# Kernel tuning notes

Hardware: AMD Instinct MI355X
Metric: run time of the kernel (lower is better)

The kernel has to match this reference:

```python
import jax, jax.numpy as jnp
import numpy as np

D = 3  # hardcoded window half-width in the module


def setup_inputs() -> dict:
    key = jax.random.key(0)
    ks = jax.random.split(key, 5)
    B, T, S = 16, 1024, 4096
    q_size, c_size, p_size = 512, 512, 512
    q = jax.random.normal(ks[0], (B, q_size, S), jnp.float32)
    c_t = jax.random.normal(ks[1], (B, T, c_size), jnp.float32)
    # torch nn.Linear weight layouts: (out_features, in_features)
    W_a = jax.random.normal(ks[2], (c_size, q_size), jnp.float32) / np.sqrt(q_size).astype(np.float32)
    W_p = jax.random.normal(ks[3], (p_size, c_size), jnp.float32) / np.sqrt(c_size).astype(np.float32)
    V_p = jax.random.normal(ks[4], (1, p_size), jnp.float32) / np.sqrt(p_size).astype(np.float32)
    return {"q": q, "c_t": c_t, "W_a": W_a, "W_p": W_p, "V_p": V_p}


def reference(q, c_t, W_a, W_p, V_p):
    B, q_size, S = q.shape
    # predictive alignment: p_t = S * sigmoid(V_p tanh(W_p c_t)) -> (B, T, 1)
    p_t = S * jax.nn.sigmoid(jnp.tanh(c_t @ W_p.T) @ V_p.T)
    # pad one NaN column at the front of the sequence, then (B, S+1, q_size)
    q_pad = jnp.pad(q, ((0, 0), (0, 0), (1, 0)), constant_values=jnp.nan).transpose(0, 2, 1)
    # window indices: clamp(long(p_t) + idx + 1, 0, S+1) % (S+1), idx in [-D, D]
    offsets = jnp.arange(-D + 1, D + 2)  # (2D+1,)
    s = jnp.clip(p_t.astype(jnp.int32) + offsets[None, None, :], 0, S + 1) % (S + 1)  # (B,T,2D+1)
    # per-batch gather of the local window: (B, T, 2D+1, q_size)
    qg = q_pad[jnp.arange(B)[:, None, None], s]
    nan_loc = jnp.isnan(qg[..., 0])  # (B, T, 2D+1)
    qg = jnp.where(nan_loc[..., None], 0.0, qg)
    # score: dot(W_a q, c_t) -> (B, T, 2D+1)
    a_t = jnp.einsum('btwq,cq,btc->btw', qg, W_a, c_t)
    a_t = jnp.where(nan_loc, -jnp.inf, a_t)
    attn = jax.nn.softmax(a_t, axis=2)
    # Gaussian decay around predicted position p_t
    gauss = jnp.exp(-2.0 * ((jnp.clip(s.astype(jnp.float32) - 1.0, 0.0, None) - p_t) / D) ** 2)
    W_attn = attn * gauss
    out = jnp.einsum('btw,btwq->btq', W_attn, qg)  # (B, T, q_size)
    return out
```

## Files before the change

### kernel.cpp

```cpp
#include <hip/hip_runtime.h>
#include <hip/hip_bf16.h>

#define BB 16
#define TT 1024
#define SS 4096
#define CS 512
#define QS 512
#define PS 512
#define NROW (BB*TT)

typedef unsigned short ushort_t;
typedef unsigned int u32;
typedef short bf16x8 __attribute__((ext_vector_type(8)));
typedef float f32x4 __attribute__((ext_vector_type(4)));

#define AS1 __attribute__((address_space(1)))
#define AS3 __attribute__((address_space(3)))

__device__ __forceinline__ void gl2l16(const void* g, void* l) {
    __builtin_amdgcn_global_load_lds((const AS1 u32*)g, (AS3 u32*)l, 16, 0, 0);
}

__device__ __forceinline__ ushort_t f2bf(float f) {
    u32 x = __float_as_uint(f);
    return (ushort_t)((x + 0x7fffu + ((x >> 16) & 1u)) >> 16);
}
__device__ __forceinline__ float bf2f(ushort_t b) {
    return __uint_as_float(((u32)b) << 16);
}

__global__ __launch_bounds__(256) void k_conv(const float* __restrict__ c,
                                              const float* __restrict__ Wa,
                                              const float* __restrict__ Wp,
                                              ushort_t* __restrict__ A,
                                              ushort_t* __restrict__ B,
                                              int* __restrict__ cnt,
                                              int* __restrict__ hist,
                                              int* __restrict__ cur) {
    const int blk = blockIdx.x;
    const int t = threadIdx.x;
    if (blk < 8192) {
        const int i = blk * 256 + t;
        const int m = i >> 7;
        const int k = (i & 127) * 4;
        float4 v = *(const float4*)(c + (size_t)m * CS + k);
        ushort4 hi, lo;
        hi.x = f2bf(v.x); lo.x = f2bf(v.x - bf2f(hi.x));
        hi.y = f2bf(v.y); lo.y = f2bf(v.y - bf2f(hi.y));
        hi.z = f2bf(v.z); lo.z = f2bf(v.z - bf2f(hi.z));
        hi.w = f2bf(v.w); lo.w = f2bf(v.w - bf2f(hi.w));
        *(ushort4*)(A + (size_t)m * 1024 + k)       = hi;
        *(ushort4*)(A + (size_t)m * 1024 + 512 + k) = lo;
    } else if (blk < 9216) {
        const int n = blk - 8192;
        if (n == 0 && t < 2) cnt[t] = 0;
        #pragma unroll
        for (int kk = 0; kk < 2; ++kk) {
            const int k = t + 256 * kk;
            float v = (n < 512) ? Wa[(size_t)k * QS + n] : Wp[(size_t)(n - 512) * CS + k];
            ushort_t hi = f2bf(v);
            ushort_t lo = f2bf(v - bf2f(hi));
            B[(size_t)n * 1024 + k]       = hi;
            B[(size_t)n * 1024 + 512 + k] = lo;
        }
    } else {
        const int idx = (blk - 9216) * 256 + t;
        if (idx < 2048) hist[idx] = 0;
        else cur[idx - 2048] = 0;
    }
}

__global__ __launch_bounds__(1024, 4) void k_gemm(const ushort_t* __restrict__ A,
                                                  const ushort_t* __restrict__ B,
                                                  const float* __restrict__ V_p,
                                                  float* __restrict__ u,
                                                  float* __restrict__ zpart) {
    __shared__ ushort_t lds[8][8192];
    const int tid = threadIdx.x;
    const int l = tid & 63;
    const int w = tid >> 6;
    const int wm = w >> 2;
    const int wn = w & 3;
    const int ln = l & 15, lh = l >> 4;

    const int orig = blockIdx.x;
    const int swz = ((orig & 7) << 5) + (orig >> 3);
    const int m0 = (swz >> 2) * 256;
    const int nt = swz & 3;
    const int n0 = nt * 256;

    const int srow = tid >> 2;
    const int scg  = tid & 3;
    const int scol0 = (scg ^ ((srow >> 1) & 3)) * 8;

    const int swzr = (lh ^ ((ln >> 1) & 3)) << 3;
    int aoffL[4], boffL[4];
    #pragma unroll
    for (int mi = 0; mi < 4; ++mi)
        aoffL[mi] = (wm * 64 + mi * 16 + ln) * 32 + swzr;
    #pragma unroll
    for (int ni = 0; ni < 4; ++ni)
        boffL[ni] = (wn * 64 + ni * 16 + ln) * 32 + swzr;

    f32x4 acc[4][4];
    #pragma unroll
    for (int a = 0; a < 4; ++a)
        #pragma unroll
        for (int b2 = 0; b2 < 4; ++b2) acc[a][b2] = (f32x4){0.f, 0.f, 0.f, 0.f};

    auto STAGE = [&](int c) {
        const int tt = c >> 2, rem = c & 3, kh = rem >> 1;
        const int blk = tt >> 3, k0 = (tt & 7) << 6;
        const ushort_t* src;
        if (rem & 1) {
            const int boff = (blk == 1) ? 512 : 0;
            src = B + (size_t)(n0 + srow) * 1024 + boff + k0 + kh * 32 + scol0;
        } else {
            const int aoff = (blk == 2) ? 512 : 0;
            src = A + (size_t)(m0 + srow) * 1024 + aoff + k0 + kh * 32 + scol0;
        }
        gl2l16(src, &lds[c & 7][tid * 8]);
    };

    #pragma unroll
    for (int c = 0; c < 4; ++c) STAGE(c);
    asm volatile("s_waitcnt vmcnt(0)" ::: "memory");
    __builtin_amdgcn_s_barrier();

    #pragma unroll 1
    for (int t = 0; t < 24; ++t) {
        if (t < 23) {
            #pragma unroll
            for (int i = 0; i < 4; ++i) STAGE(4 * t + 4 + i);
        }
        {
            const ushort_t* bA = &lds[(4 * t) & 7][0];
            const ushort_t* bB = &lds[(4 * t + 1) & 7][0];
            bf16x8 af[4], bb[4];
            #pragma unroll
            for (int mi = 0; mi < 4; ++mi)
                af[mi] = *(const bf16x8*)(bA + aoffL[mi]);
            #pragma unroll
            for (int ni = 0; ni < 4; ++ni)
                bb[ni] = *(const bf16x8*)(bB + boffL[ni]);
            __builtin_amdgcn_s_setprio(1);
            #pragma unroll
            for (int mi = 0; mi < 4; ++mi)
                #pragma unroll
                for (int ni = 0; ni < 4; ++ni)
                    acc[mi][ni] = __builtin_amdgcn_mfma_f32_16x16x32_bf16(
                        af[mi], bb[ni], acc[mi][ni], 0, 0, 0);
            __builtin_amdgcn_s_setprio(0);
        }
        {
            const ushort_t* bA = &lds[(4 * t + 2) & 7][0];
            const ushort_t* bB = &lds[(4 * t + 3) & 7][0];
            bf16x8 af[4], bb[4];
            #pragma unroll
            for (int mi = 0; mi < 4; ++mi)
                af[mi] = *(const bf16x8*)(bA + aoffL[mi]);
            #pragma unroll
            for (int ni = 0; ni < 4; ++ni)
                bb[ni] = *(const bf16x8*)(bB + boffL[ni]);
            __builtin_amdgcn_s_setprio(1);
            #pragma unroll
            for (int mi = 0; mi < 4; ++mi)
                #pragma unroll
                for (int ni = 0; ni < 4; ++ni)
                    acc[mi][ni] = __builtin_amdgcn_mfma_f32_16x16x32_bf16(
                        af[mi], bb[ni], acc[mi][ni], 0, 0, 0);
            __builtin_amdgcn_s_setprio(0);
        }
        asm volatile("s_waitcnt vmcnt(0)" ::: "memory");
        __builtin_amdgcn_s_barrier();
    }

    if (nt < 2) {
        #pragma unroll
        for (int mi = 0; mi < 4; ++mi) {
            #pragma unroll
            for (int r = 0; r < 4; ++r) {
                const int m = m0 + wm * 64 + mi * 16 + lh * 4 + r;
                float* up = u + (size_t)m * QS + nt * 256 + wn * 64 + ln;
                #pragma unroll
                for (int ni = 0; ni < 4; ++ni) up[ni * 16] = acc[mi][ni][r];
            }
        }
    } else {
        float vp[4];
        #pragma unroll
        for (int ni = 0; ni < 4; ++ni)
            vp[ni] = V_p[(nt - 2) * 256 + wn * 64 + ni * 16 + ln];
        #pragma unroll
        for (int mi = 0; mi < 4; ++mi) {
            #pragma unroll
            for (int r = 0; r < 4; ++r) {
                float sv = 0.f;
                #pragma unroll
                for (int ni = 0; ni < 4; ++ni) sv += tanhf(acc[mi][ni][r]) * vp[ni];
                sv += __shfl_xor(sv, 1, 64);
                sv += __shfl_xor(sv, 2, 64);
                sv += __shfl_xor(sv, 4, 64);
                sv += __shfl_xor(sv, 8, 64);
                if (ln == 0)
                    zpart[(size_t)(m0 + wm * 64 + mi * 16 + lh * 4 + r) * 8 +
                          (nt - 2) * 4 + wn] = sv;
            }
        }
    }
}

__global__ __launch_bounds__(256) void k_z(const float* __restrict__ zpart,
                                           float* __restrict__ pt, int* __restrict__ tr,
                                           int* __restrict__ list1, int* __restrict__ cnt1) {
    const int row = blockIdx.x * 256 + threadIdx.x;
    const float4 a = *(const float4*)(zpart + (size_t)row * 8);
    const float4 b = *(const float4*)(zpart + (size_t)row * 8 + 4);
    float z = ((a.x + a.y) + (a.z + a.w)) + ((b.x + b.y) + (b.z + b.w));
    float ptv = 4096.f / (1.f + expf(-z));
    float fr = ptv - floorf(ptv);
    pt[row] = ptv;
    tr[row] = (int)ptv;
    if (fr < 0.06f || fr > 0.94f) {
        int i = atomicAdd(cnt1, 1);
        list1[i] = row;
    }
}

__global__ __launch_bounds__(256) void k_rep1(
    const float* __restrict__ c_t, const float* __restrict__ W_p,
    const float* __restrict__ V_p, float* __restrict__ pt, int* __restrict__ tr,
    const int* __restrict__ list1, const int* __restrict__ cnt1,
    int* __restrict__ list2, int* __restrict__ cnt2)
{
    const int tid = threadIdx.x;
    const int lane = tid & 63;
    const int wid = tid >> 6;
    const int n1 = cnt1[0];
    __shared__ float cl[8][132 * 4];
    __shared__ double zl[4][8];
    __shared__ int rows_s[8];

    for (int g0 = blockIdx.x * 8; g0 < n1; g0 += gridDim.x * 8) {
        const int nr = min(8, n1 - g0);
        __syncthreads();
        if (tid < nr) rows_s[tid] = list1[g0 + tid];
        __syncthreads();
        for (int idx = tid; idx < nr * 128; idx += 256) {
            int r = idx >> 7, k = (idx & 127) * 4;
            *(float4*)&cl[r][k] = *(const float4*)(c_t + (size_t)rows_s[r] * CS + k);
        }
        __syncthreads();

        const float* wp0 = W_p + (size_t)tid * CS;
        const float* wp1 = W_p + (size_t)(tid + 256) * CS;
        f32x4 acc[2][8];
        #pragma unroll
        for (int p = 0; p < 2; ++p)
            #pragma unroll
            for (int r = 0; r < 8; ++r) acc[p][r] = (f32x4){0.f, 0.f, 0.f, 0.f};

        for (int k = 0; k < CS; k += 16) {
            f32x4 w0[4], w1[4];
            #pragma unroll
            for (int j = 0; j < 4; ++j) {
                w0[j] = *(const f32x4*)(wp0 + k + 4 * j);
                w1[j] = *(const f32x4*)(wp1 + k + 4 * j);
            }
            #pragma unroll
            for (int j = 0; j < 4; ++j) {
                #pragma unroll
                for (int r = 0; r < 8; ++r) {
                    f32x4 c4 = *(const f32x4*)&cl[r][k + 4 * j];
                    acc[0][r] += c4 * w0[j];
                    acc[1][r] += c4 * w1[j];
                }
            }
        }

        const float vp0 = V_p[tid];
        const float vp1 = V_p[tid + 256];
        double zp[8];
        #pragma unroll
        for (int r = 0; r < 8; ++r) {
            float X0 = (acc[0][r][0] + acc[0][r][1]) + (acc[0][r][2] + acc[0][r][3]);
            float X1 = (acc[1][r][0] + acc[1][r][1]) + (acc[1][r][2] + acc[1][r][3]);
            zp[r] = (double)(tanhf(X0) * vp0) + (double)(tanhf(X1) * vp1);
        }
        #pragma unroll
        for (int r = 0; r < 8; ++r) {
            double v = zp[r];
            #pragma unroll
            for (int o = 32; o > 0; o >>= 1) v += __shfl_down(v, o, 64);
            if (lane == 0) zl[wid][r] = v;
        }
        __syncthreads();
        if (tid < nr) {
            double z = (zl[0][tid] + zl[1][tid]) + (zl[2][tid] + zl[3][tid]);
            double ptv = 4096.0 / (1.0 + exp(-z));
            const int row = rows_s[tid];
            pt[row] = (float)ptv;
            tr[row] = (int)ptv;
            double fr = ptv - floor(ptv);
            if (fr < 5e-3 || fr > 0.995) {
                int i2 = atomicAdd(cnt2, 1);
                list2[i2] = row;
            }
        }
    }
}

__global__ __launch_bounds__(256) void k_rep2a(
    const float* __restrict__ c_t, const float* __restrict__ W_p,
    const float* __restrict__ V_p,
    const int* __restrict__ list2, const int* __restrict__ cnt2,
    double* __restrict__ zp2)
{
    const int tid = threadIdx.x;
    const int pl = tid & 63;
    const int kq = tid >> 6;
    const int n2 = cnt2[0];
    __shared__ float cl[CS];
    __shared__ double xsh[4][64];

    for (int i = blockIdx.x; i < n2 * 8; i += gridDim.x) {
        const int li = i >> 3;
        const int pc = i & 7;
        const int row = list2[li];
        const int p0 = pc * 64;
        __syncthreads();
        if (tid < 128)
            *(float4*)(cl + tid * 4) = *(const float4*)(c_t + (size_t)row * CS + tid * 4);
        __syncthreads();
        const float* wr = W_p + (size_t)(p0 + pl) * CS + kq * 128;
        const float* cr = cl + kq * 128;
        double Xa = 0.0, Xb = 0.0, Xc = 0.0, Xd = 0.0;
        #pragma unroll 4
        for (int k = 0; k < 128; k += 4) {
            float4 w4 = *(const float4*)(wr + k);
            float4 c4 = *(const float4*)(cr + k);
            Xa += (double)c4.x * w4.x;
            Xb += (double)c4.y * w4.y;
            Xc += (double)c4.z * w4.z;
            Xd += (double)c4.w * w4.w;
        }
        xsh[kq][pl] = (Xa + Xb) + (Xc + Xd);
        __syncthreads();
        if (tid < 64) {
            double X = (xsh[0][pl] + xsh[1][pl]) + (xsh[2][pl] + xsh[3][pl]);
            double zv = tanh(X) * (double)V_p[p0 + pl];
            #pragma unroll
            for (int o = 32; o > 0; o >>= 1) zv += __shfl_down(zv, o, 64);
            if (pl == 0) zp2[i] = zv;
        }
    }
}

__global__ __launch_bounds__(256) void k_rep2b(
    const double* __restrict__ zp2, const int* __restrict__ list2,
    const int* __restrict__ cnt2, float* __restrict__ pt, int* __restrict__ tr)
{
    const int idx = blockIdx.x * 256 + threadIdx.x;
    if (idx >= cnt2[0]) return;
    const double* zr = zp2 + (size_t)idx * 8;
    double z = 0.0;
    #pragma unroll
    for (int j = 0; j < 8; ++j) z += zr[j];
    double ptv = 4096.0 / (1.0 + exp(-z));
    const int row = list2[idx];
    pt[row] = (float)ptv;
    tr[row] = (int)ptv;
}

__global__ __launch_bounds__(256) void k_hist(const int* __restrict__ tr,
                                              int* __restrict__ hist) {
    const int row = blockIdx.x * 256 + threadIdx.x;
    const int bucket = ((row >> 10) << 7) + (tr[row] >> 5);
    atomicAdd(&hist[bucket], 1);
}

__global__ __launch_bounds__(1024) void k_scan(const int* __restrict__ hist,
                                               int* __restrict__ offA) {
    __shared__ int s0[1024], s1[1024];
    const int t = threadIdx.x;
    const int h0 = hist[2 * t];
    const int h1 = hist[2 * t + 1];
    s0[t] = h0 + h1;
    __syncthreads();
    int* src = s0;
    int* dst = s1;
    for (int off = 1; off < 1024; off <<= 1) {
        int v = src[t] + ((t >= off) ? src[t - off] : 0);
        dst[t] = v;
        __syncthreads();
        int* tmp = src; src = dst; dst = tmp;
    }
    const int excl = (t == 0) ? 0 : src[t - 1];
    offA[2 * t]     = excl;
    offA[2 * t + 1] = excl + h0;
}

__global__ __launch_bounds__(256) void k_scatter(const int* __restrict__ tr,
                                                 const int* __restrict__ offA,
                                                 int* __restrict__ cur,
                                                 int* __restrict__ list) {
    const int row = blockIdx.x * 256 + threadIdx.x;
    const int bucket = ((row >> 10) << 7) + (tr[row] >> 5);
    const int slot = atomicAdd(&cur[bucket], 1);
    list[offA[bucket] + slot] = row;
}

__global__ __launch_bounds__(512) void k_attn_f(
    const float* __restrict__ q, const float* __restrict__ u,
    const float* __restrict__ pt, const int* __restrict__ tr,
    const int* __restrict__ hist, const int* __restrict__ offA,
    const int* __restrict__ list, float* __restrict__ out)
{
    const int bucket = blockIdx.x;
    const int n = hist[bucket];
    if (n == 0) return;
    const int b = bucket >> 7;
    const int c0 = (bucket & 127) << 5;
    const int lo4 = (c0 >= 4) ? (c0 - 4) : 0;

    __shared__ float tl[39 * 512];
    const int tid = threadIdx.x;
    const float* qb = q + (size_t)b * QS * SS;

    #pragma unroll
    for (int it = 0; it < 10; ++it) {
        const int idx = tid + 512 * it;
        const int d = idx / 10;
        const int c4 = idx - d * 10;
        const int s = lo4 + c4 * 4;
        float4 v = make_float4(0.f, 0.f, 0.f, 0.f);
        if (s + 3 <= SS - 1)
            v = *(const float4*)(qb + (size_t)d * SS + s);
        const int r0 = c4 * 4;
        tl[(r0 + 0) * 512 + (d ^ (((r0 + 0) & 7) << 2))] = v.x;
        tl[(r0 + 1) * 512 + (d ^ (((r0 + 1) & 7) << 2))] = v.y;
        tl[(r0 + 2) * 512 + (d ^ (((r0 + 2) & 7) << 2))] = v.z;
        if (r0 + 3 <= 38)
            tl[(r0 + 3) * 512 + (d ^ (((r0 + 3) & 7) << 2))] = v.w;
    }
    __syncthreads();

    const int wv = tid >> 6;
    const int l = tid & 63;
    const int base = offA[bucket];

    for (int wi = wv; wi < n; wi += 8) {
        const int bt = list[base + wi];
        const float ptv = pt[bt];
        const int tn = tr[bt];

        bool val[7];
        int pos[7];
        #pragma unroll
        for (int w = 0; w < 7; ++w) {
            int sv = tn + w - 2;
            sv = sv < 0 ? 0 : (sv > SS + 1 ? SS + 1 : sv);
            if (sv == SS + 1) sv = 0;
            val[w] = (sv != 0);
            pos[w] = sv - 1;
        }

        float uv[8];
        #pragma unroll
        for (int j = 0; j < 8; ++j)
            uv[j] = u[(size_t)bt * QS + l + 64 * j];

        float qg[7][8];
        #pragma unroll
        for (int w = 0; w < 7; ++w) {
            if (val[w]) {
                const int rw = pos[w] - lo4;
                const int cc = (rw & 7) << 2;
                const float* tr0 = &tl[rw * 512];
                #pragma unroll
                for (int j = 0; j < 8; ++j)
                    qg[w][j] = tr0[(l + 64 * j) ^ cc];
            } else {
                #pragma unroll
                for (int j = 0; j < 8; ++j) qg[w][j] = 0.f;
            }
        }

        float at[7];
        #pragma unroll
        for (int w = 0; w < 7; ++w) {
            float p = 0.f;
            #pragma unroll
            for (int j = 0; j < 8; ++j) p = fmaf(qg[w][j], uv[j], p);
            #pragma unroll
            for (int o = 1; o < 64; o <<= 1) p += __shfl_xor(p, o, 64);
            at[w] = p;
        }

        float m = -1e30f;
        #pragma unroll
        for (int w = 0; w < 7; ++w) if (val[w]) m = fmaxf(m, at[w]);
        float e[7], den = 0.f;
        #pragma unroll
        for (int w = 0; w < 7; ++w) { e[w] = val[w] ? expf(at[w] - m) : 0.f; den += e[w]; }
        const float inv = 1.f / den;

        float acc[8] = {0.f, 0.f, 0.f, 0.f, 0.f, 0.f, 0.f, 0.f};
        #pragma unroll
        for (int w = 0; w < 7; ++w) {
            if (val[w]) {
                float d = ((float)pos[w] - ptv) * (1.f / 3.f);
                float wt = e[w] * inv * expf(-2.f * d * d);
                #pragma unroll
                for (int j = 0; j < 8; ++j) acc[j] = fmaf(wt, qg[w][j], acc[j]);
            }
        }

        #pragma unroll
        for (int j = 0; j < 8; ++j)
            out[(size_t)bt * QS + l + 64 * j] = acc[j];
    }
}

extern "C" void kernel_launch(void* const* d_in, const int* in_sizes, int n_in,
                              void* d_out, int out_size, void* d_ws, size_t ws_size,
                              hipStream_t stream) {
    const float* q   = (const float*)d_in[0];
    const float* c_t = (const float*)d_in[1];
    const float* W_a = (const float*)d_in[2];
    const float* W_p = (const float*)d_in[3];
    const float* V_p = (const float*)d_in[4];
    float* out = (float*)d_out;

    char* ws = (char*)d_ws;
    ushort_t* Ap   = (ushort_t*)(ws);
    ushort_t* Bp   = (ushort_t*)(ws + 33554432);
    float*    u    = (float*)  (ws + 35651584);
    float*    zp   = (float*)  (ws + 69206016);
    float*    pt   = (float*)  (ws + 69730304);
    int*      tr   = (int*)    (ws + 69795840);
    int*      l1   = (int*)    (ws + 69861376);
    int*      l2   = (int*)    (ws + 69926912);
    int*      cnt  = (int*)    (ws + 69992448);
    double*   zp2  = (double*) (ws + 69993472);
    int*      hist = (int*)    (ws + 70124544);
    int*      offA = (int*)    (ws + 70132736);
    int*      cur  = (int*)    (ws + 70140928);
    int*      list = (int*)    (ws + 70149120);

    hipLaunchKernelGGL(k_conv, dim3(9232), dim3(256), 0, stream,
                       c_t, W_a, W_p, Ap, Bp, cnt, hist, cur);
    hipLaunchKernelGGL(k_gemm, dim3(256), dim3(1024), 0, stream, Ap, Bp, V_p, u, zp);
    hipLaunchKernelGGL(k_z, dim3(64), dim3(256), 0, stream, zp, pt, tr, l1, cnt);
    hipLaunchKernelGGL(k_rep1, dim3(512), dim3(256), 0, stream,
                       c_t, W_p, V_p, pt, tr, l1, cnt, l2, cnt + 1);
    hipLaunchKernelGGL(k_rep2a, dim3(512), dim3(256), 0, stream,
                       c_t, W_p, V_p, l2, cnt + 1, zp2);
    hipLaunchKernelGGL(k_rep2b, dim3(64), dim3(256), 0, stream,
                       zp2, l2, cnt + 1, pt, tr);
    hipLaunchKernelGGL(k_hist, dim3(64), dim3(256), 0, stream, tr, hist);
    hipLaunchKernelGGL(k_scan, dim3(1), dim3(1024), 0, stream, hist, offA);
    hipLaunchKernelGGL(k_scatter, dim3(64), dim3(256), 0, stream, tr, offA, cur, list);
    hipLaunchKernelGGL(k_attn_f, dim3(2048), dim3(512), 0, stream,
                       q, u, pt, tr, hist, offA, list, out);
}
```

Baseline: 219.6 us.

## Process two buckets per block, prefetching second q tile into registers during compute

Each attention block now handles two adjacent position buckets. It loads the first q tile into LDS, issues global loads for the second tile into registers, computes the first bucket, then writes the second tile to LDS and computes it. The aim is to hide the global-load latency of the second tile behind compute and halve the grid size. In exchange, LDS use doubles to about 156 KB per block and register pressure rises from 10 float4 prefetch registers, which may reduce occupancy.

Result: slower. 236.3 us (+7.6%).

```diff
diff --git a/kernel.cpp b/kernel.cpp
--- a/kernel.cpp
+++ b/kernel.cpp
@@ -416,14 +416,16 @@
     const int* __restrict__ hist, const int* __restrict__ offA,
     const int* __restrict__ list, float* __restrict__ out)
 {
-    const int bucket = blockIdx.x;
-    const int n = hist[bucket];
-    if (n == 0) return;
-    const int b = bucket >> 7;
-    const int c0 = (bucket & 127) << 5;
-    const int lo4 = (c0 >= 4) ? (c0 - 4) : 0;
-
-    __shared__ float tl[39 * 512];
+    const int g = blockIdx.x;
+    const int n0 = hist[2 * g];
+    const int n1 = hist[2 * g + 1];
+    if ((n0 | n1) == 0) return;
+    const int b = g >> 6;
+    const int c00 = (g & 63) << 6;
+    const int lo0 = (c00 >= 4) ? (c00 - 4) : 0;
+    const int lo1 = c00 + 28;
+
+    __shared__ float tl[2][39 * 512];
     const int tid = threadIdx.x;
     const float* qb = q + (size_t)b * QS * SS;
 
@@ -432,94 +434,125 @@
         const int idx = tid + 512 * it;
         const int d = idx / 10;
         const int c4 = idx - d * 10;
-        const int s = lo4 + c4 * 4;
+        const int s = lo0 + c4 * 4;
         float4 v = make_float4(0.f, 0.f, 0.f, 0.f);
         if (s + 3 <= SS - 1)
             v = *(const float4*)(qb + (size_t)d * SS + s);
         const int r0 = c4 * 4;
-        tl[(r0 + 0) * 512 + (d ^ (((r0 + 0) & 7) << 2))] = v.x;
-        tl[(r0 + 1) * 512 + (d ^ (((r0 + 1) & 7) << 2))] = v.y;
-        tl[(r0 + 2) * 512 + (d ^ (((r0 + 2) & 7) << 2))] = v.z;
+        tl[0][(r0 + 0) * 512 + (d ^ (((r0 + 0) & 7) << 2))] = v.x;
+        tl[0][(r0 + 1) * 512 + (d ^ (((r0 + 1) & 7) << 2))] = v.y;
+        tl[0][(r0 + 2) * 512 + (d ^ (((r0 + 2) & 7) << 2))] = v.z;
         if (r0 + 3 <= 38)
-            tl[(r0 + 3) * 512 + (d ^ (((r0 + 3) & 7) << 2))] = v.w;
+            tl[0][(r0 + 3) * 512 + (d ^ (((r0 + 3) & 7) << 2))] = v.w;
+    }
+    float4 vq[10];
+    #pragma unroll
+    for (int it = 0; it < 10; ++it) {
+        const int idx = tid + 512 * it;
+        const int d = idx / 10;
+        const int c4 = idx - d * 10;
+        const int s = lo1 + c4 * 4;
+        vq[it] = make_float4(0.f, 0.f, 0.f, 0.f);
+        if (s + 3 <= SS - 1)
+            vq[it] = *(const float4*)(qb + (size_t)d * SS + s);
     }
     __syncthreads();
 
     const int wv = tid >> 6;
     const int l = tid & 63;
-    const int base = offA[bucket];
-
-    for (int wi = wv; wi < n; wi += 8) {
-        const int bt = list[base + wi];
-        const float ptv = pt[bt];
-        const int tn = tr[bt];
-
-        bool val[7];
-        int pos[7];
-        #pragma unroll
-        for (int w = 0; w < 7; ++w) {
-            int sv = tn + w - 2;
-            sv = sv < 0 ? 0 : (sv > SS + 1 ? SS + 1 : sv);
-            if (sv == SS + 1) sv = 0;
-            val[w] = (sv != 0);
-            pos[w] = sv - 1;
-        }
-
-        float uv[8];
-        #pragma unroll
-        for (int j = 0; j < 8; ++j)
-            uv[j] = u[(size_t)bt * QS + l + 64 * j];
-
-        float qg[7][8];
-        #pragma unroll
-        for (int w = 0; w < 7; ++w) {
-            if (val[w]) {
-                const int rw = pos[w] - lo4;
-                const int cc = (rw & 7) << 2;
-                const float* tr0 = &tl[rw * 512];
-                #pragma unroll
-                for (int j = 0; j < 8; ++j)
-                    qg[w][j] = tr0[(l + 64 * j) ^ cc];
-            } else {
-                #pragma unroll
-                for (int j = 0; j < 8; ++j) qg[w][j] = 0.f;
-            }
-        }
-
-        float at[7];
-        #pragma unroll
-        for (int w = 0; w < 7; ++w) {
-            float p = 0.f;
-            #pragma unroll
-            for (int j = 0; j < 8; ++j) p = fmaf(qg[w][j], uv[j], p);
-            #pragma unroll
-            for (int o = 1; o < 64; o <<= 1) p += __shfl_xor(p, o, 64);
-            at[w] = p;
-        }
-
-        float m = -1e30f;
-        #pragma unroll
-        for (int w = 0; w < 7; ++w) if (val[w]) m = fmaxf(m, at[w]);
-        float e[7], den = 0.f;
-        #pragma unroll
-        for (int w = 0; w < 7; ++w) { e[w] = val[w] ? expf(at[w] - m) : 0.f; den += e[w]; }
-        const float inv = 1.f / den;
-
-        float acc[8] = {0.f, 0.f, 0.f, 0.f, 0.f, 0.f, 0.f, 0.f};
-        #pragma unroll
-        for (int w = 0; w < 7; ++w) {
-            if (val[w]) {
-                float d = ((float)pos[w] - ptv) * (1.f / 3.f);
-                float wt = e[w] * inv * expf(-2.f * d * d);
-                #pragma unroll
-                for (int j = 0; j < 8; ++j) acc[j] = fmaf(wt, qg[w][j], acc[j]);
-            }
-        }
-
-        #pragma unroll
-        for (int j = 0; j < 8; ++j)
-            out[(size_t)bt * QS + l + 64 * j] = acc[j];
-    }
+
+    auto COMPUTE = [&](const float* tile, int bk, int lo4, int n) {
+        const int base = offA[bk];
+        for (int wi = wv; wi < n; wi += 8) {
+            const int bt = list[base + wi];
+            const float ptv = pt[bt];
+            const int tn = tr[bt];
+
+            bool val[7];
+            int pos[7];
+            #pragma unroll
+            for (int w = 0; w < 7; ++w) {
+                int sv = tn + w - 2;
+                sv = sv < 0 ? 0 : (sv > SS + 1 ? SS + 1 : sv);
+                if (sv == SS + 1) sv = 0;
+                val[w] = (sv != 0);
+                pos[w] = sv - 1;
+            }
+
+            float uv[8];
+            #pragma unroll
+            for (int j = 0; j < 8; ++j)
+                uv[j] = u[(size_t)bt * QS + l + 64 * j];
+
+            float qg[7][8];
+            #pragma unroll
+            for (int w = 0; w < 7; ++w) {
+                if (val[w]) {
+                    const int rw = pos[w] - lo4;
+                    const int cc = (rw & 7) << 2;
+                    const float* tr0 = &tile[rw * 512];
+                    #pragma unroll
+                    for (int j = 0; j < 8; ++j)
+                        qg[w][j] = tr0[(l + 64 * j) ^ cc];
+                } else {
+                    #pragma unroll
+                    for (int j = 0; j < 8; ++j) qg[w][j] = 0.f;
+                }
+            }
+
+            float at[7];
+            #pragma unroll
+            for (int w = 0; w < 7; ++w) {
+                float p = 0.f;
+                #pragma unroll
+                for (int j = 0; j < 8; ++j) p = fmaf(qg[w][j], uv[j], p);
+                #pragma unroll
+                for (int o = 1; o < 64; o <<= 1) p += __shfl_xor(p, o, 64);
+                at[w] = p;
+            }
+
+            float m = -1e30f;
+            #pragma unroll
+            for (int w = 0; w < 7; ++w) if (val[w]) m = fmaxf(m, at[w]);
+            float e[7], den = 0.f;
+            #pragma unroll
+            for (int w = 0; w < 7; ++w) { e[w] = val[w] ? expf(at[w] - m) : 0.f; den += e[w]; }
+            const float inv = 1.f / den;
+
+            float acc[8] = {0.f, 0.f, 0.f, 0.f, 0.f, 0.f, 0.f, 0.f};
+            #pragma unroll
+            for (int w = 0; w < 7; ++w) {
+                if (val[w]) {
+                    float d = ((float)pos[w] - ptv) * (1.f / 3.f);
+                    float wt = e[w] * inv * expf(-2.f * d * d);
+                    #pragma unroll
+                    for (int j = 0; j < 8; ++j) acc[j] = fmaf(wt, qg[w][j], acc[j]);
+                }
+            }
+
+            #pragma unroll
+            for (int j = 0; j < 8; ++j)
+                out[(size_t)bt * QS + l + 64 * j] = acc[j];
+        }
+    };
+
+    if (n0) COMPUTE(&tl[0][0], 2 * g, lo0, n0);
+
+    #pragma unroll
+    for (int it = 0; it < 10; ++it) {
+        const int idx = tid + 512 * it;
+        const int d = idx / 10;
+        const int c4 = idx - d * 10;
+        const int r0 = c4 * 4;
+        tl[1][(r0 + 0) * 512 + (d ^ (((r0 + 0) & 7) << 2))] = vq[it].x;
+        tl[1][(r0 + 1) * 512 + (d ^ (((r0 + 1) & 7) << 2))] = vq[it].y;
+        tl[1][(r0 + 2) * 512 + (d ^ (((r0 + 2) & 7) << 2))] = vq[it].z;
+        if (r0 + 3 <= 38)
+            tl[1][(r0 + 3) * 512 + (d ^ (((r0 + 3) & 7) << 2))] = vq[it].w;
+    }
+    __syncthreads();
+
+    if (n1) COMPUTE(&tl[1][0], 2 * g + 1, lo1, n1);
 }
 
 extern "C" void kernel_launch(void* const* d_in, const int* in_sizes, int n_in,
@@ -561,6 +594,6 @@
     hipLaunchKernelGGL(k_hist, dim3(64), dim3(256), 0, stream, tr, hist);
     hipLaunchKernelGGL(k_scan, dim3(1), dim3(1024), 0, stream, hist, offA);
     hipLaunchKernelGGL(k_scatter, dim3(64), dim3(256), 0, stream, tr, offA, cur, list);
-    hipLaunchKernelGGL(k_attn_f, dim3(2048), dim3(512), 0, stream,
+    hipLaunchKernelGGL(k_attn_f, dim3(1024), dim3(512), 0, stream,
                        q, u, pt, tr, hist, offA, list, out);
 }
```
